# Kernel tuning notes

Measured on AMD Instinct MI355X. Metric: run time of the kernel, lower is better.

The kernel has to match this reference:

```python
import jax, jax.numpy as jnp
import numpy as np

C, G, NH, NE = 640, 32, 8, 512
B, H, W, P = 8, 32, 32, 77
HD = C // NH
EPS = 1e-5


def _groupnorm(x, g, b):
    # x: (B, C, H, W); normalize over (C//G, H, W) within each of G groups
    bb, cc, hh, ww = x.shape
    xg = x.reshape(bb, G, cc // G, hh, ww)
    mu = xg.mean(axis=(2, 3, 4), keepdims=True)
    var = xg.var(axis=(2, 3, 4), keepdims=True)
    xg = (xg - mu) * jax.lax.rsqrt(var + EPS)
    return xg.reshape(bb, cc, hh, ww) * g[None, :, None, None] + b[None, :, None, None]


def _layernorm(x, g, b):
    mu = x.mean(axis=-1, keepdims=True)
    var = x.var(axis=-1, keepdims=True)
    return (x - mu) * jax.lax.rsqrt(var + EPS) * g + b


def _split_heads(t):
    # (B, S, C) -> (B, NH, S, HD)
    bb, ss, _ = t.shape
    return t.reshape(bb, ss, NH, HD).transpose(0, 2, 1, 3)


def _attn(q, k, v):
    # q,k,v: (B, NH, S, HD) — manual softmax(q k^T / sqrt(d)) v, as in the source
    scores = jnp.einsum('bhqd,bhkd->bhqk', q, k) / (HD ** 0.5)
    probs = jax.nn.softmax(scores, axis=-1)
    out = jnp.einsum('bhqk,bhkd->bhqd', probs, v)
    bb = q.shape[0]
    return out.transpose(0, 2, 1, 3).reshape(bb, q.shape[2], C)


def unet_attention_fwd(x, p, gn_g, gn_b, ci_w, ci_b, ln1_g, ln1_b,
                       qkv_w, qkv_b, saw_w, saw_b, ln2_g, ln2_b,
                       caq_w, caq_b, cak_w, cak_b, cav_w, cav_b, caw_w, caw_b,
                       ln3_g, ln3_b, g1_w, g1_b, g2_w, g2_b, co_w, co_b):
    residue_long = x
    h = _groupnorm(x, gn_g, gn_b)
    # conv_input: 1x1 conv == per-pixel linear; ci_w: (C_in, C_out)
    h = jnp.einsum('bihw,io->bohw', h, ci_w) + ci_b[None, :, None, None]
    bb, cc, hh, ww = h.shape
    h = h.reshape(bb, cc, hh * ww).transpose(0, 2, 1)  # (B, HW, C)

    # self attention
    res = h
    t = _layernorm(h, ln1_g, ln1_b)
    qkv = t @ qkv_w + qkv_b
    q, k, v = jnp.split(qkv, 3, axis=-1)
    t = _attn(_split_heads(q), _split_heads(k), _split_heads(v))
    h = res + (t @ saw_w + saw_b)

    # cross attention (prompt p: (B, 77, NE))
    res = h
    t = _layernorm(h, ln2_g, ln2_b)
    q = t @ caq_w + caq_b
    k = p @ cak_w + cak_b
    v = p @ cav_w + cav_b
    t = _attn(_split_heads(q), _split_heads(k), _split_heads(v))
    h = res + (t @ caw_w + caw_b)

    # GEGLU MLP (exact GELU, matching torch F.gelu default)
    res = h
    t = _layernorm(h, ln3_g, ln3_b)
    proj = t @ g1_w + g1_b  # (B, HW, 8C)
    a, gate = jnp.split(proj, 2, axis=-1)
    t = a * jax.nn.gelu(gate, approximate=False)
    h = res + (t @ g2_w + g2_b)

    h = h.transpose(0, 2, 1).reshape(bb, cc, hh, ww)
    out = jnp.einsum('bihw,io->bohw', h, co_w) + co_b[None, :, None, None]
    return out + residue_long


def setup_inputs() -> dict:
    keys = jax.random.split(jax.random.key(0), 20)
    ki = iter(keys)
    s = 0.02

    def w(shape):
        return jax.random.normal(next(ki), shape, jnp.float32) * s

    return {
        'x': jax.random.normal(next(ki), (B, C, H, W), jnp.float32),
        'p': jax.random.normal(next(ki), (B, P, NE), jnp.float32),
        'gn_g': jnp.ones((C,), jnp.float32), 'gn_b': jnp.zeros((C,), jnp.float32),
        'ci_w': w((C, C)), 'ci_b': jnp.zeros((C,), jnp.float32),
        'ln1_g': jnp.ones((C,), jnp.float32), 'ln1_b': jnp.zeros((C,), jnp.float32),
        'qkv_w': w((C, 3 * C)), 'qkv_b': jnp.zeros((3 * C,), jnp.float32),
        'saw_w': w((C, C)), 'saw_b': jnp.zeros((C,), jnp.float32),
        'ln2_g': jnp.ones((C,), jnp.float32), 'ln2_b': jnp.zeros((C,), jnp.float32),
        'caq_w': w((C, C)), 'caq_b': jnp.zeros((C,), jnp.float32),
        'cak_w': w((NE, C)), 'cak_b': jnp.zeros((C,), jnp.float32),
        'cav_w': w((NE, C)), 'cav_b': jnp.zeros((C,), jnp.float32),
        'caw_w': w((C, C)), 'caw_b': jnp.zeros((C,), jnp.float32),
        'ln3_g': jnp.ones((C,), jnp.float32), 'ln3_b': jnp.zeros((C,), jnp.float32),
        'g1_w': w((C, 8 * C)), 'g1_b': jnp.zeros((8 * C,), jnp.float32),
        'g2_w': w((4 * C, C)), 'g2_b': jnp.zeros((C,), jnp.float32),
        'co_w': w((C, C)), 'co_b': jnp.zeros((C,), jnp.float32),
    }


def reference(x, p, gn_g, gn_b, ci_w, ci_b, ln1_g, ln1_b,
              qkv_w, qkv_b, saw_w, saw_b, ln2_g, ln2_b,
              caq_w, caq_b, cak_w, cak_b, cav_w, cav_b, caw_w, caw_b,
              ln3_g, ln3_b, g1_w, g1_b, g2_w, g2_b, co_w, co_b):
    return unet_attention_fwd(x, p, gn_g, gn_b, ci_w, ci_b, ln1_g, ln1_b,
                              qkv_w, qkv_b, saw_w, saw_b, ln2_g, ln2_b,
                              caq_w, caq_b, cak_w, cak_b, cav_w, cav_b, caw_w, caw_b,
                              ln3_g, ln3_b, g1_w, g1_b, g2_w, g2_b, co_w, co_b)
```

## Files before the change

kernel.cpp:

```cpp
#include <hip/hip_runtime.h>
#include <math.h>

typedef unsigned short u16;
typedef __attribute__((ext_vector_type(8))) short short8;
typedef __attribute__((ext_vector_type(4))) float f32x4;

#define DI static __device__ __forceinline__

DI float bf2f(u16 u) { union { unsigned u; float f; } c; c.u = (unsigned)u << 16; return c.f; }
DI u16 f2bf(float f) {
  union { float f; unsigned u; } c; c.f = f;
  unsigned r = c.u + 0x7fffu + ((c.u >> 16) & 1u);
  return (u16)(r >> 16);
}

DI void gload16(const u16* g, u16* l) {
  __builtin_amdgcn_global_load_lds(
      (const __attribute__((address_space(1))) unsigned int*)g,
      (__attribute__((address_space(3))) unsigned int*)l, 16, 0, 0);
}

struct PrepDesc { const float* src; u16* dst; int K, N, nbx, boff, perm; };
struct PrepArgs { PrepDesc d[10]; };

__global__ __launch_bounds__(256) void prep_all(PrepArgs a) {
  int bid = blockIdx.x;
  int i = 0;
  while (i < 9 && bid >= a.d[i + 1].boff) i++;
  const PrepDesc D = a.d[i];
  int rel = bid - D.boff;
  int bx = rel % D.nbx, by = rel / D.nbx;
  int K = D.K, N = D.N;
  __shared__ float tile[32][33];
  int k0 = by * 32, n0 = bx * 32;
  int tid = threadIdx.x;
  int ni = tid & 31, ki8 = tid >> 5;
  for (int q = 0; q < 4; q++) {
    int k = ki8 + q * 8;
    tile[k][ni] = D.src[(size_t)(k0 + k) * N + n0 + ni];
  }
  __syncthreads();
  int kj = tid & 31, nj8 = tid >> 5;
  for (int q = 0; q < 4; q++) {
    int n = nj8 + q * 8;
    int nold = n0 + n;
    int rowp = nold;
    if (D.perm) {
      rowp = (nold < 2560) ? ((nold >> 5) * 64 + (nold & 31))
                           : (((nold - 2560) >> 5) * 64 + 32 + (nold & 31));
    }
    D.dst[(size_t)rowp * K + k0 + kj] = f2bf(tile[kj][n]);
  }
}

__global__ __launch_bounds__(256) void conv_bf16(const float* __restrict__ in,
                                                 u16* __restrict__ out, long n) {
  long i = (long)blockIdx.x * 256 + threadIdx.x;
  if (i < n) out[i] = f2bf(in[i]);
}

__global__ __launch_bounds__(256) void gn_stats(const float* __restrict__ x,
                                                float* __restrict__ mean_o,
                                                float* __restrict__ rstd_o) {
  int bg = blockIdx.x;
  const float4* p = (const float4*)(x + (size_t)bg * 20480);
  float s = 0.f, sq = 0.f;
  for (int i = threadIdx.x; i < 5120; i += 256) {
    float4 v = p[i];
    s += v.x + v.y + v.z + v.w;
    sq += v.x * v.x + v.y * v.y + v.z * v.z + v.w * v.w;
  }
  for (int off = 1; off < 64; off <<= 1) { s += __shfl_xor(s, off); sq += __shfl_xor(sq, off); }
  __shared__ float ps[4], pq[4];
  int w = threadIdx.x >> 6;
  if ((threadIdx.x & 63) == 0) { ps[w] = s; pq[w] = sq; }
  __syncthreads();
  if (threadIdx.x == 0) {
    float S = ps[0] + ps[1] + ps[2] + ps[3];
    float Q = pq[0] + pq[1] + pq[2] + pq[3];
    float mu = S / 20480.f;
    float var = Q / 20480.f - mu * mu;
    mean_o[bg] = mu;
    rstd_o[bg] = rsqrtf(var + 1e-5f);
  }
}

__global__ __launch_bounds__(256) void gn_apply(const float* __restrict__ x,
                                                const float* __restrict__ mean_,
                                                const float* __restrict__ rstd_,
                                                const float* __restrict__ g,
                                                const float* __restrict__ bb,
                                                u16* __restrict__ out) {
  __shared__ float tile[32][33];
  int b = blockIdx.z, c0 = blockIdx.y * 32, s0 = blockIdx.x * 32;
  int tid = threadIdx.x;
  int si = tid & 31, ci8 = tid >> 5;
  for (int i = 0; i < 4; i++) {
    int c = c0 + ci8 + i * 8;
    int gg = c / 20;
    float mu = mean_[b * 32 + gg], rs = rstd_[b * 32 + gg];
    float v = x[((size_t)b * 640 + c) * 1024 + s0 + si];
    tile[ci8 + i * 8][si] = (v - mu) * rs * g[c] + bb[c];
  }
  __syncthreads();
  int cj = tid & 31, sj8 = tid >> 5;
  for (int i = 0; i < 4; i++) {
    int sj = sj8 + i * 8;
    out[((size_t)b * 1024 + s0 + sj) * 640 + c0 + cj] = f2bf(tile[cj][sj]);
  }
}

__global__ __launch_bounds__(256) void ln_kernel(const float* __restrict__ in,
                                                 const float* __restrict__ g,
                                                 const float* __restrict__ bb,
                                                 u16* __restrict__ out) {
  int t = blockIdx.x * 4 + (threadIdx.x >> 6);
  int lane = threadIdx.x & 63;
  const float* row = in + (size_t)t * 640;
  float xv[10], s = 0.f, sq = 0.f;
  for (int j = 0; j < 10; j++) {
    xv[j] = row[lane + j * 64];
    s += xv[j];
    sq += xv[j] * xv[j];
  }
  for (int off = 1; off < 64; off <<= 1) { s += __shfl_xor(s, off); sq += __shfl_xor(sq, off); }
  float mu = s * (1.f / 640.f);
  float var = sq * (1.f / 640.f) - mu * mu;
  float rstd = rsqrtf(var + 1e-5f);
  for (int j = 0; j < 10; j++) {
    int c = lane + j * 64;
    out[(size_t)t * 640 + c] = f2bf((xv[j] - mu) * rstd * g[c] + bb[c]);
  }
}


DI const short8* fragp(const u16* unit, int row, int g4) {
  int off = row * 64 + g4 * 16;
  off ^= ((off >> 7) & 3) << 4;
  return (const short8*)((const char*)unit + off);
}

template <int MODE>
__global__ __launch_bounds__(512, 1) void gemm256(const u16* __restrict__ A,
                                                  const u16* __restrict__ Bt,
                                                  const float* __restrict__ bias,
                                                  void* outp, const float* res,
                                                  int M, int N, int K) {
  __shared__ __align__(16) u16 As[4][2][4096];
  __shared__ __align__(16) u16 Bs[4][2][4096];
  const int tid = threadIdx.x;
  const int lane = tid & 63, wid = tid >> 6;
  const int wm = wid >> 2, wn = wid & 3;
  const int rq = lane & 15, g4 = lane >> 4;
  const int m0 = blockIdx.x * 256, n0 = blockIdx.y * 256;

  int off0 = tid * 16;
  int soff = off0 ^ (((off0 >> 7) & 3) << 4);
  const int srow = soff >> 6;
  const int skb = soff & 63;

  f32x4 acc[8][4] = {};

  const int nt = K >> 5;

#define STG_TILE(kt, bufi)                                                        \
  {                                                                               \
    gload16(A + (size_t)(m0 + srow) * K + (kt)*32 + (skb >> 1),                   \
            &As[bufi][0][0] + tid * 8);                                           \
    gload16(A + (size_t)(m0 + 128 + srow) * K + (kt)*32 + (skb >> 1),             \
            &As[bufi][1][0] + tid * 8);                                           \
    gload16(Bt + (size_t)(n0 + srow) * K + (kt)*32 + (skb >> 1),                  \
            &Bs[bufi][0][0] + tid * 8);                                           \
    gload16(Bt + (size_t)(n0 + 128 + srow) * K + (kt)*32 + (skb >> 1),            \
            &Bs[bufi][1][0] + tid * 8);                                           \
  }

#define COMPUTE(bufi)                                                             \
  {                                                                               \
    const u16* Au = &As[bufi][wm][0];                                             \
    const u16* Bu = &Bs[bufi][wn >> 1][0];                                        \
    short8 af[8], bf[4];                                                          \
    _Pragma("unroll") for (int i = 0; i < 8; i++)                                 \
        af[i] = *fragp(Au, i * 16 + rq, g4);                                      \
    _Pragma("unroll") for (int j = 0; j < 4; j++)                                 \
        bf[j] = *fragp(Bu, (wn & 1) * 64 + j * 16 + rq, g4);                      \
    __builtin_amdgcn_s_setprio(1);                                                \
    _Pragma("unroll") for (int i = 0; i < 8; i++)                                 \
        _Pragma("unroll") for (int j = 0; j < 4; j++)                             \
            acc[i][j] =                                                           \
        __builtin_amdgcn_mfma_f32_16x16x32_bf16(af[i], bf[j], acc[i][j], 0, 0, 0);\
    __builtin_amdgcn_s_setprio(0);                                                \
  }

#define BAR asm volatile("s_barrier" ::: "memory")

  STG_TILE(0, 0);
  STG_TILE(1, 1);
  STG_TILE(2, 2);

  int t = 0;
  for (; t + 3 < nt; t++) {
    STG_TILE(t + 3, (t + 3) & 3);
    asm volatile("s_waitcnt vmcnt(12)" ::: "memory");
    BAR;
    COMPUTE(t & 3);
    BAR;
  }
  for (; t < nt; t++) {
    int rem = nt - 1 - t;
    if (rem >= 2)
      asm volatile("s_waitcnt vmcnt(8)" ::: "memory");
    else if (rem == 1)
      asm volatile("s_waitcnt vmcnt(4)" ::: "memory");
    else
      asm volatile("s_waitcnt vmcnt(0)" ::: "memory");
    BAR;
    COMPUTE(t & 3);
    BAR;
  }

  if (MODE == 5) {
#pragma unroll
    for (int mf = 0; mf < 8; mf++) {
      int mb = m0 + wm * 128 + mf * 16 + g4 * 4;
#pragma unroll
      for (int j = 0; j < 2; j++) {
        int n = n0 + wn * 64 + j * 16 + rq;
        int c = (n >> 6) * 32 + (n & 31);
        float ba = bias[c];
        float bg = bias[2560 + c];
#pragma unroll
        for (int r = 0; r < 4; r++) {
          float a = acc[mf][j][r] + ba;
          float gt = acc[mf][j + 2][r] + bg;
          float gl = 0.5f * gt * (1.f + erff(gt * 0.70710678f));
          ((u16*)outp)[(size_t)(mb + r) * 2560 + c] = f2bf(a * gl);
        }
      }
    }
  } else {
#pragma unroll
    for (int mf = 0; mf < 8; mf++) {
#pragma unroll
      for (int j = 0; j < 4; j++) {
        int n = n0 + wn * 64 + j * 16 + rq;
        if (n >= N) continue;
        float bv = bias[n];
        int mb = m0 + wm * 128 + mf * 16 + g4 * 4;
        f32x4 v = acc[mf][j];
#pragma unroll
        for (int r = 0; r < 4; r++) {
          size_t o = (size_t)(mb + r) * N + n;
          ((u16*)outp)[o] = f2bf(v[r] + bv);
        }
      }
    }
  }
  (void)res;
#undef STG_TILE
#undef COMPUTE
#undef BAR
}

template <int MODE>
__global__ __launch_bounds__(256) void gemm_bt(const u16* __restrict__ A,
                                               const u16* __restrict__ Bt,
                                               const float* __restrict__ bias,
                                               void* outp, const float* res,
                                               int M, int N, int K) {
  __shared__ __align__(16) u16 As[2][128 * 32];
  __shared__ __align__(16) u16 Bs[2][128 * 32];
  const int tid = threadIdx.x;
  const int lane = tid & 63, wid = tid >> 6;
  const int wm = wid >> 1, wn = wid & 1;
  const int m0 = blockIdx.x * 128, n0 = blockIdx.y * 128;
  const int rq = lane & 15, g4 = lane >> 4;

  const int srow = tid >> 2;
  const int scol = tid & 3;
  int gmA0 = m0 + srow;        if (gmA0 >= M) gmA0 = M - 1;
  int gmA1 = m0 + 64 + srow;   if (gmA1 >= M) gmA1 = M - 1;
  const u16* gA0 = A + (size_t)gmA0 * K + scol * 8;
  const u16* gA1 = A + (size_t)gmA1 * K + scol * 8;
  const u16* gB0 = Bt + (size_t)(n0 + srow) * K + scol * 8;
  const u16* gB1 = Bt + (size_t)(n0 + 64 + srow) * K + scol * 8;
  u16* lA0 = &As[0][srow * 32 + scol * 8];
  u16* lA1 = &As[0][(64 + srow) * 32 + scol * 8];
  u16* lB0 = &Bs[0][srow * 32 + scol * 8];
  u16* lB1 = &Bs[0][(64 + srow) * 32 + scol * 8];

  f32x4 acc[4][4] = {};

  auto STAGE = [&](int buf, int k0) {
    int o = buf * (128 * 32);
    gload16(gA0 + k0, lA0 + o);
    gload16(gA1 + k0, lA1 + o);
    gload16(gB0 + k0, lB0 + o);
    gload16(gB1 + k0, lB1 + o);
  };
  auto COMPUTE = [&](int buf) {
    short8 af[4], bfr[4];
    for (int i = 0; i < 4; i++)
      af[i] = *(const short8*)&As[buf][(wm * 64 + i * 16 + rq) * 32 + g4 * 8];
    for (int j = 0; j < 4; j++)
      bfr[j] = *(const short8*)&Bs[buf][(wn * 64 + j * 16 + rq) * 32 + g4 * 8];
    __builtin_amdgcn_s_setprio(1);
    for (int i = 0; i < 4; i++)
      for (int j = 0; j < 4; j++)
        acc[i][j] = __builtin_amdgcn_mfma_f32_16x16x32_bf16(af[i], bfr[j], acc[i][j], 0, 0, 0);
    __builtin_amdgcn_s_setprio(0);
  };

  const int nk = K >> 5;
  STAGE(0, 0);
  int cur = 0;
  for (int t = 0; t < nk - 1; t++) {
    STAGE(cur ^ 1, (t + 1) << 5);
    asm volatile("s_waitcnt vmcnt(4)" ::: "memory");
    __builtin_amdgcn_s_barrier();
    COMPUTE(cur);
    __builtin_amdgcn_s_barrier();
    cur ^= 1;
  }
  asm volatile("s_waitcnt vmcnt(0)" ::: "memory");
  __builtin_amdgcn_s_barrier();
  COMPUTE(cur);

  for (int j = 0; j < 4; j++) {
    int n = n0 + wn * 64 + j * 16 + rq;
    float bv = bias[n];
    for (int i = 0; i < 4; i++) {
      int mb = m0 + wm * 64 + i * 16 + g4 * 4;
      f32x4 v = acc[i][j];
      if (MODE == 3) {
        int b = mb >> 10, sp = mb & 1023;
        size_t o = ((size_t)b * 640 + n) * 1024 + sp;
        f32x4 xv = *(const f32x4*)(res + o);
        f32x4 ov;
        for (int r = 0; r < 4; r++) ov[r] = v[r] + bv + xv[r];
        *(f32x4*)((float*)outp + o) = ov;
      } else {
        for (int r = 0; r < 4; r++) {
          int m = mb + r;
          if (m >= M) break;
          size_t o = (size_t)m * N + n;
          float val = v[r] + bv;
          if (MODE == 0)
            ((float*)outp)[o] = val;
          else if (MODE == 1)
            ((u16*)outp)[o] = f2bf(val);
          else if (MODE == 2)
            ((float*)outp)[o] = val + res[o];
          else
            ((u16*)outp)[o] = f2bf(val + res[o]);
        }
      }
    }
  }
}

__global__ __launch_bounds__(256) void attn_kernel(const u16* __restrict__ Qb, int ldq, long qbs,
                                                   const u16* __restrict__ Kb, int ldk, long kbs,
                                                   const u16* __restrict__ Vb,
                                                   u16* __restrict__ Ob, int ldo, long obs,
                                                   int Sk, float scale) {
  __shared__ __align__(16) u16 Ks[64 * 96];
  __shared__ __align__(16) u16 Vt[80 * 64];
  __shared__ __align__(16) u16 Ps[4][16 * 72];
  const short8 zero = {0, 0, 0, 0, 0, 0, 0, 0};
  const int tid = threadIdx.x;
  const int lane = tid & 63, w = tid >> 6;
  const int rq = lane & 15, g4 = lane >> 4;
  const int b = blockIdx.z, h = blockIdx.y;
  const u16* Q = Qb + (size_t)b * qbs + h * 80;
  const u16* Kp = Kb + (size_t)b * kbs + h * 80;
  const u16* Vp = Vb + (size_t)b * kbs + h * 80;
  u16* Op = Ob + (size_t)b * obs + h * 80;
  const int q0 = blockIdx.x * 64 + w * 16;
  const float Af = scale * 1.44269504f;

  short8 qa[3];
#pragma unroll
  for (int kk = 0; kk < 3; kk++) {
    int d = kk * 32 + g4 * 8;
    qa[kk] = (d < 80) ? *(const short8*)(Q + (size_t)(q0 + rq) * ldq + d) : zero;
  }
  f32x4 oacc[5] = {};
  float m_run = -1e30f, l_run = 0.f;

  const int nkt = (Sk + 63) >> 6;
  for (int kt = 0; kt < nkt; kt++) {
    const int kbase = kt * 64;
    for (int s = tid; s < 768; s += 256) {
      int row = s / 12, c = s % 12;
      int kidx = kbase + row;
      short8 v = zero;
      if (c < 10 && kidx < Sk) v = *(const short8*)(Kp + (size_t)kidx * ldk + c * 8);
      int byte = row * 192 + c * 16;
      byte ^= (row & 7) << 4;
      *(short8*)((char*)Ks + byte) = v;
    }
    for (int s = tid; s < 320; s += 256) {
      int k2 = (s & 31) * 2, c = s >> 5;
      int k0i = kbase + k2;
      short8 v0 = zero, v1 = zero;
      if (k0i < Sk) v0 = *(const short8*)(Vp + (size_t)k0i * ldk + c * 8);
      if (k0i + 1 < Sk) v1 = *(const short8*)(Vp + (size_t)(k0i + 1) * ldk + c * 8);
#pragma unroll
      for (int jj = 0; jj < 8; jj++) {
        int d = c * 8 + jj;
        unsigned cm = (unsigned)(u16)v0[jj] | ((unsigned)(u16)v1[jj] << 16);
        int byte = d * 128 + k2 * 2;
        byte ^= (d & 7) << 4;
        *(unsigned*)((char*)Vt + byte) = cm;
      }
    }
    __syncthreads();

    f32x4 sc[4] = {};
#pragma unroll
    for (int n = 0; n < 4; n++)
#pragma unroll
      for (int kk = 0; kk < 3; kk++) {
        int row = n * 16 + rq;
        int byte = row * 192 + (kk * 32 + g4 * 8) * 2;
        byte ^= (rq & 7) << 4;
        short8 kb = *(const short8*)((const char*)Ks + byte);
        sc[n] = __builtin_amdgcn_mfma_f32_16x16x32_bf16(kb, qa[kk], sc[n], 0, 0, 0);
      }
    const bool full = (kbase + 64 <= Sk);
    if (!full) {
#pragma unroll
      for (int n = 0; n < 4; n++)
#pragma unroll
        for (int r = 0; r < 4; r++)
          if (kbase + n * 16 + g4 * 4 + r >= Sk) sc[n][r] = -1e30f;
    }
    float t0 = fmaxf(fmaxf(sc[0][0], sc[0][1]), fmaxf(sc[0][2], sc[0][3]));
    float t1 = fmaxf(fmaxf(sc[1][0], sc[1][1]), fmaxf(sc[1][2], sc[1][3]));
    float t2 = fmaxf(fmaxf(sc[2][0], sc[2][1]), fmaxf(sc[2][2], sc[2][3]));
    float t3 = fmaxf(fmaxf(sc[3][0], sc[3][1]), fmaxf(sc[3][2], sc[3][3]));
    float tm = fmaxf(fmaxf(t0, t1), fmaxf(t2, t3));
    tm = fmaxf(tm, __shfl_xor(tm, 16));
    tm = fmaxf(tm, __shfl_xor(tm, 32));
    if (!__all(tm <= m_run + 48.0f)) {
      float mn = fmaxf(m_run, tm);
      float sf = exp2f(Af * (m_run - mn));
      m_run = mn;
      l_run *= sf;
      float sfo[4];
#pragma unroll
      for (int r = 0; r < 4; r++) sfo[r] = __shfl(sf, g4 * 4 + r);
#pragma unroll
      for (int nn = 0; nn < 5; nn++)
#pragma unroll
        for (int r = 0; r < 4; r++) oacc[nn][r] *= sfo[r];
    }
    const float Am = Af * m_run;
    float rs0 = 0.f, rs1 = 0.f;
#pragma unroll
    for (int n = 0; n < 4; n++) {
      float p0 = exp2f(fmaf(Af, sc[n][0], -Am));
      float p1 = exp2f(fmaf(Af, sc[n][1], -Am));
      float p2 = exp2f(fmaf(Af, sc[n][2], -Am));
      float p3 = exp2f(fmaf(Af, sc[n][3], -Am));
      sc[n][0] = p0; sc[n][1] = p1; sc[n][2] = p2; sc[n][3] = p3;
      rs0 += p0 + p1;
      rs1 += p2 + p3;
    }
    float rsum = rs0 + rs1;
    rsum += __shfl_xor(rsum, 16);
    rsum += __shfl_xor(rsum, 32);
    l_run += rsum;
#pragma unroll
    for (int n = 0; n < 4; n++) {
      unsigned pk0, pk1;
      asm("v_cvt_pk_bf16_f32 %0, %1, %2" : "=v"(pk0) : "v"(sc[n][0]), "v"(sc[n][1]));
      asm("v_cvt_pk_bf16_f32 %0, %1, %2" : "=v"(pk1) : "v"(sc[n][2]), "v"(sc[n][3]));
      int base = rq * 72 + n * 16 + g4 * 4;
      *(unsigned*)&Ps[w][base] = pk0;
      *(unsigned*)&Ps[w][base + 2] = pk1;
    }
    __builtin_amdgcn_s_setprio(1);
#pragma unroll
    for (int s = 0; s < 2; s++) {
      short8 pa = *(const short8*)&Ps[w][rq * 72 + s * 32 + g4 * 8];
#pragma unroll
      for (int nn = 0; nn < 5; nn++) {
        int row = nn * 16 + rq;
        int byte = row * 128 + (s * 32 + g4 * 8) * 2;
        byte ^= (rq & 7) << 4;
        short8 vb = *(const short8*)((const char*)Vt + byte);
        oacc[nn] = __builtin_amdgcn_mfma_f32_16x16x32_bf16(pa, vb, oacc[nn], 0, 0, 0);
      }
    }
    __builtin_amdgcn_s_setprio(0);
    __syncthreads();
  }
  float lo[4];
#pragma unroll
  for (int r = 0; r < 4; r++) lo[r] = 1.0f / __shfl(l_run, g4 * 4 + r);
#pragma unroll
  for (int nn = 0; nn < 5; nn++)
#pragma unroll
    for (int r = 0; r < 4; r++)
      Op[(size_t)(q0 + g4 * 4 + r) * ldo + nn * 16 + rq] = f2bf(oacc[nn][r] * lo[r]);
}

extern "C" void kernel_launch(void* const* d_in, const int* in_sizes, int n_in,
                              void* d_out, int out_size, void* d_ws, size_t ws_size,
                              hipStream_t stream) {
  (void)in_sizes; (void)n_in; (void)out_size; (void)ws_size;
  const float* x = (const float*)d_in[0];
  const float* p = (const float*)d_in[1];
  const float* gn_g = (const float*)d_in[2];
  const float* gn_b = (const float*)d_in[3];
  const float* ci_w = (const float*)d_in[4];
  const float* ci_b = (const float*)d_in[5];
  const float* ln1_g = (const float*)d_in[6];
  const float* ln1_b = (const float*)d_in[7];
  const float* qkv_w = (const float*)d_in[8];
  const float* qkv_b = (const float*)d_in[9];
  const float* saw_w = (const float*)d_in[10];
  const float* saw_b = (const float*)d_in[11];
  const float* ln2_g = (const float*)d_in[12];
  const float* ln2_b = (const float*)d_in[13];
  const float* caq_w = (const float*)d_in[14];
  const float* caq_b = (const float*)d_in[15];
  const float* cak_w = (const float*)d_in[16];
  const float* cak_b = (const float*)d_in[17];
  const float* cav_w = (const float*)d_in[18];
  const float* cav_b = (const float*)d_in[19];
  const float* caw_w = (const float*)d_in[20];
  const float* caw_b = (const float*)d_in[21];
  const float* ln3_g = (const float*)d_in[22];
  const float* ln3_b = (const float*)d_in[23];
  const float* g1_w = (const float*)d_in[24];
  const float* g1_b = (const float*)d_in[25];
  const float* g2_w = (const float*)d_in[26];
  const float* g2_b = (const float*)d_in[27];
  const float* co_w = (const float*)d_in[28];
  const float* co_b = (const float*)d_in[29];
  float* out = (float*)d_out;

  char* ws = (char*)d_ws;
  size_t off = 0;
  auto alloc = [&](size_t bytes) {
    size_t o = off;
    off += (bytes + 255) & ~(size_t)255;
    return o;
  };
  u16* WCI = (u16*)(ws + alloc((size_t)768 * 640 * 2));
  u16* WQKV = (u16*)(ws + alloc((size_t)2048 * 640 * 2));
  u16* WSAW = (u16*)(ws + alloc((size_t)768 * 640 * 2));
  u16* WCAQ = (u16*)(ws + alloc((size_t)768 * 640 * 2));
  u16* WCAK = (u16*)(ws + alloc((size_t)640 * 512 * 2));
  u16* WCAV = (u16*)(ws + alloc((size_t)640 * 512 * 2));
  u16* WCAW = (u16*)(ws + alloc((size_t)768 * 640 * 2));
  u16* WG1 = (u16*)(ws + alloc((size_t)5120 * 640 * 2));
  u16* WG2 = (u16*)(ws + alloc((size_t)768 * 2560 * 2));
  u16* WCO = (u16*)(ws + alloc((size_t)768 * 640 * 2));
  u16* X = (u16*)(ws + alloc((size_t)8192 * 640 * 2));
  u16* Y = (u16*)(ws + alloc((size_t)8192 * 640 * 2));
  float* F1 = (float*)(ws + alloc((size_t)8192 * 640 * 4));
  u16* QKV = (u16*)(ws + alloc((size_t)8192 * 1920 * 2));
  u16* PBF = (u16*)(ws + alloc((size_t)616 * 512 * 2));
  u16* KC = (u16*)(ws + alloc((size_t)616 * 640 * 2));
  u16* VC = (u16*)(ws + alloc((size_t)616 * 640 * 2));
  u16* TG = (u16*)(ws + alloc((size_t)8192 * 2560 * 2));
  float* GNM = (float*)(ws + alloc(256 * 4));
  float* GNR = (float*)(ws + alloc(256 * 4));

  PrepArgs pa;
  int boff = 0;
  auto addw = [&](int idx, const float* src, u16* dst, int K, int N, int perm) {
    pa.d[idx].src = src; pa.d[idx].dst = dst;
    pa.d[idx].K = K; pa.d[idx].N = N;
    pa.d[idx].nbx = N / 32; pa.d[idx].boff = boff; pa.d[idx].perm = perm;
    boff += (N / 32) * (K / 32);
  };
  addw(0, ci_w, WCI, 640, 640, 0);
  addw(1, qkv_w, WQKV, 640, 1920, 0);
  addw(2, saw_w, WSAW, 640, 640, 0);
  addw(3, caq_w, WCAQ, 640, 640, 0);
  addw(4, cak_w, WCAK, 512, 640, 0);
  addw(5, cav_w, WCAV, 512, 640, 0);
  addw(6, caw_w, WCAW, 640, 640, 0);
  addw(7, g1_w, WG1, 640, 5120, 1);
  addw(8, g2_w, WG2, 2560, 640, 0);
  addw(9, co_w, WCO, 640, 640, 0);
  prep_all<<<boff, 256, 0, stream>>>(pa);
  conv_bf16<<<1232, 256, 0, stream>>>(p, PBF, (long)616 * 512);

  gn_stats<<<256, 256, 0, stream>>>(x, GNM, GNR);
  gn_apply<<<dim3(32, 20, 8), 256, 0, stream>>>(x, GNM, GNR, gn_g, gn_b, X);

  const float scale = 0.11180339887498949f;

  gemm_bt<0><<<dim3(64, 5), 256, 0, stream>>>(X, WCI, ci_b, F1, nullptr, 8192, 640, 640);
  ln_kernel<<<2048, 256, 0, stream>>>(F1, ln1_g, ln1_b, Y);
  gemm256<1><<<dim3(32, 8), 512, 0, stream>>>(Y, WQKV, qkv_b, QKV, nullptr, 8192, 1920, 640);
  attn_kernel<<<dim3(16, 8, 8), 256, 0, stream>>>(QKV, 1920, (long)1024 * 1920,
                                                  QKV + 640, 1920, (long)1024 * 1920,
                                                  QKV + 1280, X, 640, (long)1024 * 640,
                                                  1024, scale);
  gemm_bt<2><<<dim3(64, 5), 256, 0, stream>>>(X, WSAW, saw_b, F1, F1, 8192, 640, 640);
  ln_kernel<<<2048, 256, 0, stream>>>(F1, ln2_g, ln2_b, Y);
  gemm_bt<1><<<dim3(64, 5), 256, 0, stream>>>(Y, WCAQ, caq_b, X, nullptr, 8192, 640, 640);
  gemm_bt<1><<<dim3(5, 5), 256, 0, stream>>>(PBF, WCAK, cak_b, KC, nullptr, 616, 640, 512);
  gemm_bt<1><<<dim3(5, 5), 256, 0, stream>>>(PBF, WCAV, cav_b, VC, nullptr, 616, 640, 512);
  attn_kernel<<<dim3(16, 8, 8), 256, 0, stream>>>(X, 640, (long)1024 * 640,
                                                  KC, 640, (long)77 * 640,
                                                  VC, Y, 640, (long)1024 * 640,
                                                  77, scale);
  gemm_bt<2><<<dim3(64, 5), 256, 0, stream>>>(Y, WCAW, caw_b, F1, F1, 8192, 640, 640);
  ln_kernel<<<2048, 256, 0, stream>>>(F1, ln3_g, ln3_b, X);
  gemm256<5><<<dim3(32, 20), 512, 0, stream>>>(X, WG1, g1_b, TG, nullptr, 8192, 5120, 640);
  gemm_bt<4><<<dim3(64, 5), 256, 0, stream>>>(TG, WG2, g2_b, X, F1, 8192, 640, 2560);
  gemm_bt<3><<<dim3(64, 5), 256, 0, stream>>>(X, WCO, co_b, out, x, 8192, 640, 640);
}
```

Before: 490.7 us.

## Split 256x256 GEMM main loop into two phases interleaving loads with MFMA

Restructures the gemm256 main loop so each K-tile is processed in two half-phases. The first phase reads the A and B fragments for the first half of the rows and issues the A prefetch for tile t+3. The second phase reads the remaining A fragments, reuses the B fragments, and issues the B prefetch. This spreads global-to-LDS loads and LDS reads across the MFMA work and roughly halves fragment register pressure. In exchange it doubles the barrier count per tile and adds explicit lgkmcnt waits. The epilogue handling assumes at least three K tiles.

```diff
diff --git a/kernel.cpp b/kernel.cpp
--- a/kernel.cpp
+++ b/kernel.cpp
@@ -146,78 +146,89 @@
                                                   const float* __restrict__ bias,
                                                   void* outp, const float* res,
                                                   int M, int N, int K) {
-  __shared__ __align__(16) u16 As[4][2][4096];
-  __shared__ __align__(16) u16 Bs[4][2][4096];
+  __shared__ __align__(16) u16 As[4][8192];
+  __shared__ __align__(16) u16 Bs[4][8192];
   const int tid = threadIdx.x;
   const int lane = tid & 63, wid = tid >> 6;
   const int wm = wid >> 2, wn = wid & 3;
   const int rq = lane & 15, g4 = lane >> 4;
   const int m0 = blockIdx.x * 256, n0 = blockIdx.y * 256;
 
-  int off0 = tid * 16;
-  int soff = off0 ^ (((off0 >> 7) & 3) << 4);
-  const int srow = soff >> 6;
-  const int skb = soff & 63;
+  int D0 = tid * 16;
+  int so = D0 ^ (((D0 >> 7) & 3) << 4);
+  const int srow = so >> 6;
+  const int sk16 = (so & 63) >> 1;
 
   f32x4 acc[8][4] = {};
-
   const int nt = K >> 5;
 
-#define STG_TILE(kt, bufi)                                                        \
-  {                                                                               \
-    gload16(A + (size_t)(m0 + srow) * K + (kt)*32 + (skb >> 1),                   \
-            &As[bufi][0][0] + tid * 8);                                           \
-    gload16(A + (size_t)(m0 + 128 + srow) * K + (kt)*32 + (skb >> 1),             \
-            &As[bufi][1][0] + tid * 8);                                           \
-    gload16(Bt + (size_t)(n0 + srow) * K + (kt)*32 + (skb >> 1),                  \
-            &Bs[bufi][0][0] + tid * 8);                                           \
-    gload16(Bt + (size_t)(n0 + 128 + srow) * K + (kt)*32 + (skb >> 1),            \
-            &Bs[bufi][1][0] + tid * 8);                                           \
-  }
-
-#define COMPUTE(bufi)                                                             \
-  {                                                                               \
-    const u16* Au = &As[bufi][wm][0];                                             \
-    const u16* Bu = &Bs[bufi][wn >> 1][0];                                        \
-    short8 af[8], bf[4];                                                          \
-    _Pragma("unroll") for (int i = 0; i < 8; i++)                                 \
-        af[i] = *fragp(Au, i * 16 + rq, g4);                                      \
-    _Pragma("unroll") for (int j = 0; j < 4; j++)                                 \
-        bf[j] = *fragp(Bu, (wn & 1) * 64 + j * 16 + rq, g4);                      \
-    __builtin_amdgcn_s_setprio(1);                                                \
-    _Pragma("unroll") for (int i = 0; i < 8; i++)                                 \
-        _Pragma("unroll") for (int j = 0; j < 4; j++)                             \
-            acc[i][j] =                                                           \
-        __builtin_amdgcn_mfma_f32_16x16x32_bf16(af[i], bf[j], acc[i][j], 0, 0, 0);\
-    __builtin_amdgcn_s_setprio(0);                                                \
-  }
-
+#define STG_A(kt)                                                              \
+  {                                                                            \
+    gload16(A + (size_t)(m0 + srow) * K + (kt)*32 + sk16,                      \
+            &As[(kt) & 3][0] + tid * 8);                                       \
+    gload16(A + (size_t)(m0 + 128 + srow) * K + (kt)*32 + sk16,                \
+            &As[(kt) & 3][4096] + tid * 8);                                    \
+  }
+#define STG_B(kt)                                                              \
+  {                                                                            \
+    gload16(Bt + (size_t)(n0 + srow) * K + (kt)*32 + sk16,                     \
+            &Bs[(kt) & 3][0] + tid * 8);                                       \
+    gload16(Bt + (size_t)(n0 + 128 + srow) * K + (kt)*32 + sk16,               \
+            &Bs[(kt) & 3][4096] + tid * 8);                                    \
+  }
 #define BAR asm volatile("s_barrier" ::: "memory")
 
-  STG_TILE(0, 0);
-  STG_TILE(1, 1);
-  STG_TILE(2, 2);
-
+#define PH1(T, DO_STG)                                                         \
+  {                                                                            \
+    const u16* Au = &As[(T) & 3][0];                                           \
+    const u16* Bu = &Bs[(T) & 3][0];                                           \
+    _Pragma("unroll") for (int i = 0; i < 4; i++)                              \
+        af[i] = *fragp(Au, wm * 128 + i * 16 + rq, g4);                        \
+    _Pragma("unroll") for (int j = 0; j < 4; j++)                              \
+        bf[j] = *fragp(Bu, wn * 64 + j * 16 + rq, g4);                         \
+    if (DO_STG) STG_A((T) + 3);                                                \
+    BAR;                                                                       \
+    asm volatile("s_waitcnt lgkmcnt(0)" ::: "memory");                         \
+    __builtin_amdgcn_s_setprio(1);                                             \
+    _Pragma("unroll") for (int i = 0; i < 4; i++)                              \
+        _Pragma("unroll") for (int j = 0; j < 4; j++)                          \
+            acc[i][j] =                                                        \
+        __builtin_amdgcn_mfma_f32_16x16x32_bf16(af[i], bf[j], acc[i][j], 0, 0, 0); \
+    __builtin_amdgcn_s_setprio(0);                                             \
+    BAR;                                                                       \
+  }
+
+#define PH2(T, DO_STG, WSTR)                                                   \
+  {                                                                            \
+    const u16* Au = &As[(T) & 3][0];                                           \
+    _Pragma("unroll") for (int i = 0; i < 4; i++)                              \
+        af[i] = *fragp(Au, wm * 128 + 64 + i * 16 + rq, g4);                   \
+    if (DO_STG) STG_B((T) + 3);                                                \
+    asm volatile(WSTR ::: "memory");                                           \
+    BAR;                                                                       \
+    asm volatile("s_waitcnt lgkmcnt(0)" ::: "memory");                         \
+    __builtin_amdgcn_s_setprio(1);                                             \
+    _Pragma("unroll") for (int i = 0; i < 4; i++)                              \
+        _Pragma("unroll") for (int j = 0; j < 4; j++)                          \
+            acc[4 + i][j] =                                                    \
+        __builtin_amdgcn_mfma_f32_16x16x32_bf16(af[i], bf[j], acc[4 + i][j], 0, 0, 0); \
+    __builtin_amdgcn_s_setprio(0);                                             \
+    BAR;                                                                       \
+  }
+
+  STG_A(0); STG_B(0); STG_A(1); STG_B(1); STG_A(2); STG_B(2);
+  asm volatile("s_waitcnt vmcnt(8)" ::: "memory");
+  BAR;
+
+  short8 af[4], bf[4];
   int t = 0;
-  for (; t + 3 < nt; t++) {
-    STG_TILE(t + 3, (t + 3) & 3);
-    asm volatile("s_waitcnt vmcnt(12)" ::: "memory");
-    BAR;
-    COMPUTE(t & 3);
-    BAR;
-  }
-  for (; t < nt; t++) {
-    int rem = nt - 1 - t;
-    if (rem >= 2)
-      asm volatile("s_waitcnt vmcnt(8)" ::: "memory");
-    else if (rem == 1)
-      asm volatile("s_waitcnt vmcnt(4)" ::: "memory");
-    else
-      asm volatile("s_waitcnt vmcnt(0)" ::: "memory");
-    BAR;
-    COMPUTE(t & 3);
-    BAR;
-  }
+  for (; t < nt - 3; t++) {
+    PH1(t, true);
+    PH2(t, true, "s_waitcnt vmcnt(8)");
+  }
+  PH1(t, false); PH2(t, false, "s_waitcnt vmcnt(4)"); t++;
+  PH1(t, false); PH2(t, false, "s_waitcnt vmcnt(0)"); t++;
+  PH1(t, false); PH2(t, false, "s_nop 0");
 
   if (MODE == 5) {
 #pragma unroll
@@ -257,8 +268,10 @@
     }
   }
   (void)res;
-#undef STG_TILE
-#undef COMPUTE
+#undef STG_A
+#undef STG_B
+#undef PH1
+#undef PH2
 #undef BAR
 }
 
```

Measured after the change: 489.8 us. No clear change (-0.2%).
